# Optimization experiments

Measured on AMD Instinct MI355X. Metric: run time of the kernel, lower is better.

## Reference

```python
import jax, jax.numpy as jnp
import numpy as np

_SAMPLING_EPS = 1e-5
EOS_PROB_RATIO = 100.0
MIN_PROB_THRESHOLD = 0.001
MIX_RATIO = 0.5
EOS_TOKEN_ID = 2


def setup_inputs() -> dict:
    key = jax.random.key(0)
    k1, k2, k3, k4 = jax.random.split(key, 4)
    B, V = 256, 128000
    logits = jax.random.normal(k1, (B, V), dtype=jnp.float32) * 3.0
    # keep temperature away from 0 so the random-sampling path is exercised
    temperature = 0.2 + 1.3 * jax.random.uniform(k2, (B,), dtype=jnp.float32)
    top_p = 0.5 + 0.5 * jax.random.uniform(k3, (B,), dtype=jnp.float32)
    token_lengths = jax.random.randint(k4, (V,), 0, 20).astype(jnp.int32)
    return {
        "logits": logits,
        "temperature": temperature,
        "top_p": top_p,
        "token_lengths": token_lengths,
        "top_k": 50,
    }


def _apply_top_k_top_p(logits, top_k, top_p):
    """vLLM-style: ascending sort, top-k threshold, top-p cumulative mask, scatter back."""
    idx = jnp.argsort(logits, axis=-1)  # ascending
    lsort = jnp.take_along_axis(logits, idx, axis=-1)
    V = logits.shape[-1]
    # top-k: keep only the last top_k (largest) entries
    kth = lsort[:, V - top_k][:, None]
    lsort = jnp.where(lsort < kth, -jnp.inf, lsort)
    # top-p: mask low-cumulative-probability prefix (ascending order)
    probs = jax.nn.softmax(lsort, axis=-1)
    csum = jnp.cumsum(probs, axis=-1)
    pmask = csum <= (1.0 - top_p[:, None])
    pmask = pmask.at[:, -1].set(False)  # always keep the top token
    lsort = jnp.where(pmask, -jnp.inf, lsort)
    # scatter back to original token order
    inv = jnp.argsort(idx, axis=-1)
    return jnp.take_along_axis(lsort, inv, axis=-1)


def _longest_word_sample(logits, token_lengths, k, mix_ratio, eos_token_id):
    topk_logits, topk_idx = jax.lax.top_k(logits, k)  # [B,k]
    prob = jax.nn.softmax(topk_logits, axis=-1)
    lens = token_lengths[jnp.clip(topk_idx, 0, token_lengths.shape[0] - 1)].astype(jnp.float32)
    length_score = jax.nn.softmax(lens, axis=-1)
    mix = (1.0 - mix_ratio) * prob + mix_ratio * length_score
    mix = jnp.where(prob >= MIN_PROB_THRESHOLD, mix, -jnp.inf)
    # EOS threshold rule
    eos_in_topk = (topk_idx == eos_token_id) & jnp.isfinite(topk_logits)
    rows_with_eos = eos_in_topk.any(axis=-1, keepdims=True)
    eos_prob = jnp.sum(prob * eos_in_topk, axis=-1, keepdims=True)
    eos_thresh = jnp.maximum(eos_prob / EOS_PROB_RATIO, 0.005)
    valid = prob >= eos_thresh
    mix = jnp.where(valid | ~rows_with_eos, mix, -jnp.inf)
    best = jnp.argmax(mix, axis=-1)  # [B]
    chosen = jnp.take_along_axis(topk_idx, best[:, None], axis=-1)[:, 0]
    return chosen


def reference(logits, temperature, top_p, token_lengths, top_k):
    greedy = jnp.argmax(logits, axis=-1)
    scaled = logits / temperature[:, None]
    filtered = _apply_top_k_top_p(scaled, top_k, top_p)
    rnd = _longest_word_sample(filtered, token_lengths, top_k, MIX_RATIO, EOS_TOKEN_ID)
    sampled = jnp.where(temperature < _SAMPLING_EPS, greedy, rnd)
    return sampled.astype(jnp.int32)
```

## Files before the change

### kernel.cpp

```cpp
#include <hip/hip_runtime.h>
#include <stdint.h>
#include <math.h>

typedef unsigned long long u64;

#define K1_THREADS 512
#define K1_WAVES 8
#define K1_BATCH 4
#define SPLIT 4
#define NBINS 2048
#define BIN_SHIFT 21
#define CAND_MAX 1024
#define MAXK 64

__device__ __forceinline__ uint32_t fkey(float f) {
    uint32_t b = __float_as_uint(f);
    return b ^ (uint32_t)(((int32_t)b >> 31) | 0x80000000);
}
__device__ __forceinline__ float fval(uint32_t k) {
    uint32_t b = (k & 0x80000000u) ? (k & 0x7FFFFFFFu) : ~k;
    return __uint_as_float(b);
}

#define INSB(vf, gidx) do {                                                    \
    u64 c_ = ((u64)fkey(vf) << 32) | (uint32_t)~(uint32_t)(gidx);              \
    bool g0_ = c_ > t0; u64 n0_ = g0_ ? c_ : t0; c_ = g0_ ? t0 : c_; t0 = n0_; \
    bool g1_ = c_ > t1; u64 n1_ = g1_ ? c_ : t1; c_ = g1_ ? t1 : c_; t1 = n1_; \
    bool g2_ = c_ > t2; u64 n2_ = g2_ ? c_ : t2; c_ = g2_ ? t2 : c_; t2 = n2_; \
    bool g3_ = c_ > t3; u64 n3_ = g3_ ? c_ : t3; c_ = g3_ ? t3 : c_; t3 = n3_; \
    uint32_t dk_ = (uint32_t)(c_ >> 32);                                       \
    dkey = (dk_ > dkey) ? dk_ : dkey;                                          \
} while (0)

__global__ __launch_bounds__(K1_THREADS, 8) void topk_slice_kernel(
    const float* __restrict__ logits,
    const int* __restrict__ top_k_ptr,
    u64* __restrict__ ws, int V)
{
    const int row = blockIdx.x / SPLIT;
    const int sl  = blockIdx.x % SPLIT;
    const int tid = threadIdx.x;
    const int lane = tid & 63;
    const int wid  = tid >> 6;
    int K = *top_k_ptr;
    if (K < 1) K = 1;
    if (K > MAXK) K = MAXK;

    __shared__ u64 s_cand4[K1_THREADS * 4];
    __shared__ uint32_t s_hist[NBINS];
    __shared__ u64 s_cand[CAND_MAX];
    __shared__ u64 s_top[MAXK];
    __shared__ uint32_t s_wsum[K1_WAVES], s_wtail[K1_WAVES];
    __shared__ int s_T, s_cnt;

    for (int i = tid; i < NBINS; i += K1_THREADS) s_hist[i] = 0u;
    if (tid == 0) s_cnt = 0;

    const float* rowbase = logits + (size_t)row * (size_t)V;
    const float4* rowp = reinterpret_cast<const float4*>(rowbase);
    const int nv = V >> 2;
    const int snf = (nv + SPLIT - 1) / SPLIT;
    const int f0 = sl * snf;
    const int f1 = (f0 + snf < nv) ? (f0 + snf) : nv;

    u64 t0 = 0ull, t1 = 0ull, t2 = 0ull, t3 = 0ull;
    uint32_t dkey = 0u;
    const int step = K1_THREADS * K1_BATCH;
    const int niter = (f1 - f0) / step;

    for (int it = 0; it < niter; ++it) {
        const int j0 = f0 + it * step + tid;
        float4 x[K1_BATCH];
        #pragma unroll
        for (int b = 0; b < K1_BATCH; ++b) x[b] = rowp[j0 + b * K1_THREADS];
        #pragma unroll
        for (int b = 0; b < K1_BATCH; ++b) {
            const int g = (j0 + b * K1_THREADS) << 2;
            INSB(x[b].x, g + 0);
            INSB(x[b].y, g + 1);
            INSB(x[b].z, g + 2);
            INSB(x[b].w, g + 3);
        }
    }
    for (int j = f0 + niter * step + tid; j < f1; j += K1_THREADS) {
        float4 x = rowp[j];
        const int g = j << 2;
        INSB(x.x, g + 0);
        INSB(x.y, g + 1);
        INSB(x.z, g + 2);
        INSB(x.w, g + 3);
    }
    __syncthreads();

    s_cand4[tid * 4 + 0] = t0;
    s_cand4[tid * 4 + 1] = t1;
    s_cand4[tid * 4 + 2] = t2;
    s_cand4[tid * 4 + 3] = t3;
    atomicAdd(&s_hist[(uint32_t)(t0 >> 32) >> BIN_SHIFT], 1u);
    atomicAdd(&s_hist[(uint32_t)(t1 >> 32) >> BIN_SHIFT], 1u);
    atomicAdd(&s_hist[(uint32_t)(t2 >> 32) >> BIN_SHIFT], 1u);
    atomicAdd(&s_hist[(uint32_t)(t3 >> 32) >> BIN_SHIFT], 1u);
    __syncthreads();

    const int CH = NBINS / K1_THREADS;
    uint32_t cs = 0;
    {
        const int b0 = tid * CH;
        #pragma unroll
        for (int b = 0; b < CH; ++b) cs += s_hist[b0 + b];
    }
    uint32_t suf = cs;
    #pragma unroll
    for (int off = 1; off < 64; off <<= 1) {
        uint32_t o = __shfl_down(suf, off, 64);
        suf += (lane + off < 64) ? o : 0u;
    }
    if (lane == 0) s_wsum[wid] = suf;
    __syncthreads();
    if (wid == 0 && lane < K1_WAVES) {
        uint32_t t = s_wsum[lane];
        uint32_t s = t;
        #pragma unroll
        for (int off = 1; off < K1_WAVES; off <<= 1) {
            uint32_t o = __shfl_down(s, off, 64);
            s += (lane + off < K1_WAVES) ? o : 0u;
        }
        s_wtail[lane] = s - t;
    }
    __syncthreads();
    {
        uint32_t sufg = suf + s_wtail[wid];
        uint32_t sufn = sufg - cs;
        if (sufg >= (uint32_t)K && sufn < (uint32_t)K) {
            uint32_t acc = sufn;
            int T = tid * CH;
            for (int b = tid * CH + CH - 1; b >= tid * CH; --b) {
                acc += s_hist[b];
                if (acc >= (uint32_t)K) { T = b; break; }
            }
            s_T = T;
        }
    }
    __syncthreads();

    const uint32_t T = (uint32_t)s_T;
    #pragma unroll
    for (int r = 0; r < 4; ++r) {
        u64 c = s_cand4[tid * 4 + r];
        if (((uint32_t)(c >> 32) >> BIN_SHIFT) >= T) {
            int p = atomicAdd(&s_cnt, 1);
            if (p < CAND_MAX) s_cand[p] = c;
        }
    }
    __syncthreads();

    {
        const int M = (s_cnt < CAND_MAX) ? s_cnt : CAND_MAX;
        for (int t = tid; t < M; t += K1_THREADS) {
            const u64 mine = s_cand[t];
            int rank = 0;
            for (int j = 0; j < M; ++j) rank += (s_cand[j] > mine) ? 1 : 0;
            if (rank < MAXK) s_top[rank] = mine;
        }
    }
    __syncthreads();

    const u64 kth = s_top[K - 1];
    const int bad = (dkey >= (uint32_t)(kth >> 32)) ? 1 : 0;
    if (__syncthreads_or(bad)) {
        if (tid == 0) s_cnt = 0;
        __syncthreads();
        const int e0 = f0 << 2;
        const int e1 = f1 << 2;
        for (int e = e0 + tid; e < e1; e += K1_THREADS) {
            u64 p = ((u64)fkey(rowbase[e]) << 32) | (uint32_t)~(uint32_t)e;
            if (p >= kth) {
                int q = atomicAdd(&s_cnt, 1);
                if (q < CAND_MAX) s_cand[q] = p;
            }
        }
        __syncthreads();
        const int M2 = (s_cnt < CAND_MAX) ? s_cnt : CAND_MAX;
        for (int t = tid; t < M2; t += K1_THREADS) {
            const u64 mine = s_cand[t];
            int rank = 0;
            for (int j = 0; j < M2; ++j) rank += (s_cand[j] > mine) ? 1 : 0;
            if (rank < MAXK) s_top[rank] = mine;
        }
        __syncthreads();
    }

    if (tid < K) ws[(size_t)blockIdx.x * MAXK + tid] = s_top[tid];
}

__global__ __launch_bounds__(256) void merge_sampler_kernel(
    const u64* __restrict__ ws,
    const float* __restrict__ temperature,
    const float* __restrict__ top_p,
    const int* __restrict__ token_lengths,
    const int* __restrict__ top_k_ptr,
    int* __restrict__ out, int V)
{
    const int row = blockIdx.x;
    const int tid = threadIdx.x;
    int K = *top_k_ptr;
    if (K < 1) K = 1;
    if (K > MAXK) K = MAXK;
    const int M = SPLIT * K;

    __shared__ u64 s_cand[SPLIT * MAXK];
    __shared__ float s_vals[MAXK];
    __shared__ int s_idx[MAXK], s_slot[MAXK];

    if (tid < M) {
        const int s = tid / K, k = tid - s * K;
        s_cand[tid] = ws[(size_t)(row * SPLIT + s) * MAXK + k];
    }
    __syncthreads();

    if (tid < M) {
        const u64 mine = s_cand[tid];
        int rank = 0;
        for (int j = 0; j < M; ++j) rank += (s_cand[j] > mine) ? 1 : 0;
        if (rank < MAXK) {
            s_idx[rank]  = (int)(~(uint32_t)mine);
            s_vals[rank] = fval((uint32_t)(mine >> 32));
        }
    }
    __syncthreads();

    if (tid >= 64) return;

    const float temp = temperature[row];
    const float tp   = top_p[row];

    const float a0 = s_vals[0] / temp;
    float e = 0.f;
    int myidx = -1;
    if (tid < K) {
        myidx = s_idx[tid];
        e = expf(s_vals[tid] / temp - a0);
    }
    float sum = e;
    #pragma unroll
    for (int off = 1; off < 64; off <<= 1) sum += __shfl_xor(sum, off, 64);
    const float p1 = e / sum;

    float csf = p1;
    #pragma unroll
    for (int off = 1; off < 64; off <<= 1) {
        float o = __shfl_down(csf, off, 64);
        csf += (tid + off < 64) ? o : 0.f;
    }
    const float lim = 1.0f - tp;
    const bool keep = (tid < K) && (tid == 0 || csf > lim);
    const int S = __popcll(__ballot(keep));

    float e2 = (tid < S) ? e : 0.f;
    float sum2 = e2;
    #pragma unroll
    for (int off = 1; off < 64; off <<= 1) sum2 += __shfl_xor(sum2, off, 64);
    const float p2 = e2 / sum2;

    const bool is_eos = (tid < S) && (myidx == 2);
    float eosp = is_eos ? p2 : 0.f;
    #pragma unroll
    for (int off = 1; off < 64; off <<= 1) eosp += __shfl_xor(eosp, off, 64);
    const bool has_eos = (__ballot(is_eos) != 0ull);
    const float eth = fmaxf(eosp / 100.0f, 0.005f);

    if (tid < S) s_slot[tid] = myidx;
    __builtin_amdgcn_wave_barrier();
    if (tid == 0) {
        u64 m0 = 0ull, m1 = 0ull;
        for (int i = 0; i < S; ++i) {
            int id = s_idx[i];
            if (id < 64) m0 |= 1ull << id;
            else if (id < 128) m1 |= 1ull << (id - 64);
        }
        int nxt = 0;
        for (int i = S; i < K; ++i) {
            while ((nxt < 64) ? ((m0 >> nxt) & 1ull) : ((m1 >> (nxt - 64)) & 1ull)) nxt++;
            s_slot[i] = nxt++;
        }
    }
    __builtin_amdgcn_wave_barrier();

    float len = -INFINITY;
    if (tid < K) {
        int id = s_slot[tid];
        id = (id < 0) ? 0 : ((id >= V) ? V - 1 : id);
        len = (float)token_lengths[id];
    }
    float lmax = len;
    #pragma unroll
    for (int off = 1; off < 64; off <<= 1) lmax = fmaxf(lmax, __shfl_xor(lmax, off, 64));
    float el = (tid < K) ? expf(len - lmax) : 0.f;
    float lsum = el;
    #pragma unroll
    for (int off = 1; off < 64; off <<= 1) lsum += __shfl_xor(lsum, off, 64);
    const float ls = el / lsum;

    float mix = -INFINITY;
    if (tid < S) {
        mix = 0.5f * p2 + 0.5f * ls;
        if (!(p2 >= 0.001f)) mix = -INFINITY;
        if (has_eos && !(p2 >= eth)) mix = -INFINITY;
    }
    float bm = mix; int bi = tid;
    #pragma unroll
    for (int off = 1; off < 64; off <<= 1) {
        float om = __shfl_xor(bm, off, 64);
        int   oi = __shfl_xor(bi, off, 64);
        if (om > bm || (om == bm && oi < bi)) { bm = om; bi = oi; }
    }

    if (tid == 0) {
        int chosen = s_slot[bi];
        if (temp < 1e-5f) chosen = s_idx[0];
        out[row] = chosen;
    }
}

extern "C" void kernel_launch(void* const* d_in, const int* in_sizes, int n_in,
                              void* d_out, int out_size, void* d_ws, size_t ws_size,
                              hipStream_t stream) {
    const float* logits        = (const float*)d_in[0];
    const float* temperature   = (const float*)d_in[1];
    const float* top_p         = (const float*)d_in[2];
    const int*   token_lengths = (const int*)d_in[3];
    const int*   top_k_ptr     = (const int*)d_in[4];
    int* outp = (int*)d_out;
    u64* ws   = (u64*)d_ws;

    const int B = in_sizes[1];
    const int V = in_sizes[3];

    topk_slice_kernel<<<B * SPLIT, K1_THREADS, 0, stream>>>(logits, top_k_ptr, ws, V);
    merge_sampler_kernel<<<B, 256, 0, stream>>>(ws, temperature, top_p,
                                                token_lengths, top_k_ptr, outp, V);
}
```

Baseline: 49.64 us.

## Replace per-thread top-4 insertion with sampled histogram threshold and filter pass

Each block now builds a histogram from a small strided sample of its slice and picks a bin threshold so that about SAMPLE_TARGET sampled values lie above it. A single streaming pass then pushes every element above the threshold into a shared candidate list, and the threshold is adjusted one bin at a time and the pass repeated if too few or too many candidates appear. This removes the register sorting network run on every element, at the risk of several full re-scans when the sample is unrepresentative. After the retry limit, rows can end up with fewer than K candidates or with the list truncated, which could drop true top-k entries.

```diff
diff --git a/kernel.cpp b/kernel.cpp
--- a/kernel.cpp
+++ b/kernel.cpp
@@ -10,7 +10,8 @@
 #define SPLIT 4
 #define NBINS 2048
 #define BIN_SHIFT 21
-#define CAND_MAX 1024
+#define SAMPLE_TARGET 16
+#define CAND_MAX 2048
 #define MAXK 64
 
 __device__ __forceinline__ uint32_t fkey(float f) {
@@ -21,16 +22,6 @@
     uint32_t b = (k & 0x80000000u) ? (k & 0x7FFFFFFFu) : ~k;
     return __uint_as_float(b);
 }
-
-#define INSB(vf, gidx) do {                                                    \
-    u64 c_ = ((u64)fkey(vf) << 32) | (uint32_t)~(uint32_t)(gidx);              \
-    bool g0_ = c_ > t0; u64 n0_ = g0_ ? c_ : t0; c_ = g0_ ? t0 : c_; t0 = n0_; \
-    bool g1_ = c_ > t1; u64 n1_ = g1_ ? c_ : t1; c_ = g1_ ? t1 : c_; t1 = n1_; \
-    bool g2_ = c_ > t2; u64 n2_ = g2_ ? c_ : t2; c_ = g2_ ? t2 : c_; t2 = n2_; \
-    bool g3_ = c_ > t3; u64 n3_ = g3_ ? c_ : t3; c_ = g3_ ? t3 : c_; t3 = n3_; \
-    uint32_t dk_ = (uint32_t)(c_ >> 32);                                       \
-    dkey = (dk_ > dkey) ? dk_ : dkey;                                          \
-} while (0)
 
 __global__ __launch_bounds__(K1_THREADS, 8) void topk_slice_kernel(
     const float* __restrict__ logits,
@@ -46,7 +37,6 @@
     if (K < 1) K = 1;
     if (K > MAXK) K = MAXK;
 
-    __shared__ u64 s_cand4[K1_THREADS * 4];
     __shared__ uint32_t s_hist[NBINS];
     __shared__ u64 s_cand[CAND_MAX];
     __shared__ u64 s_top[MAXK];
@@ -54,7 +44,6 @@
     __shared__ int s_T, s_cnt;
 
     for (int i = tid; i < NBINS; i += K1_THREADS) s_hist[i] = 0u;
-    if (tid == 0) s_cnt = 0;
 
     const float* rowbase = logits + (size_t)row * (size_t)V;
     const float4* rowp = reinterpret_cast<const float4*>(rowbase);
@@ -62,44 +51,19 @@
     const int snf = (nv + SPLIT - 1) / SPLIT;
     const int f0 = sl * snf;
     const int f1 = (f0 + snf < nv) ? (f0 + snf) : nv;
-
-    u64 t0 = 0ull, t1 = 0ull, t2 = 0ull, t3 = 0ull;
-    uint32_t dkey = 0u;
-    const int step = K1_THREADS * K1_BATCH;
-    const int niter = (f1 - f0) / step;
-
-    for (int it = 0; it < niter; ++it) {
-        const int j0 = f0 + it * step + tid;
-        float4 x[K1_BATCH];
-        #pragma unroll
-        for (int b = 0; b < K1_BATCH; ++b) x[b] = rowp[j0 + b * K1_THREADS];
-        #pragma unroll
-        for (int b = 0; b < K1_BATCH; ++b) {
-            const int g = (j0 + b * K1_THREADS) << 2;
-            INSB(x[b].x, g + 0);
-            INSB(x[b].y, g + 1);
-            INSB(x[b].z, g + 2);
-            INSB(x[b].w, g + 3);
-        }
-    }
-    for (int j = f0 + niter * step + tid; j < f1; j += K1_THREADS) {
+    __syncthreads();
+
+    {
+        int stride = (f1 - f0) / K1_THREADS;
+        if (stride < 1) stride = 1;
+        int j = f0 + tid * stride;
+        if (j >= f1) j = f1 - 1;
         float4 x = rowp[j];
-        const int g = j << 2;
-        INSB(x.x, g + 0);
-        INSB(x.y, g + 1);
-        INSB(x.z, g + 2);
-        INSB(x.w, g + 3);
-    }
-    __syncthreads();
-
-    s_cand4[tid * 4 + 0] = t0;
-    s_cand4[tid * 4 + 1] = t1;
-    s_cand4[tid * 4 + 2] = t2;
-    s_cand4[tid * 4 + 3] = t3;
-    atomicAdd(&s_hist[(uint32_t)(t0 >> 32) >> BIN_SHIFT], 1u);
-    atomicAdd(&s_hist[(uint32_t)(t1 >> 32) >> BIN_SHIFT], 1u);
-    atomicAdd(&s_hist[(uint32_t)(t2 >> 32) >> BIN_SHIFT], 1u);
-    atomicAdd(&s_hist[(uint32_t)(t3 >> 32) >> BIN_SHIFT], 1u);
+        atomicAdd(&s_hist[fkey(x.x) >> BIN_SHIFT], 1u);
+        atomicAdd(&s_hist[fkey(x.y) >> BIN_SHIFT], 1u);
+        atomicAdd(&s_hist[fkey(x.z) >> BIN_SHIFT], 1u);
+        atomicAdd(&s_hist[fkey(x.w) >> BIN_SHIFT], 1u);
+    }
     __syncthreads();
 
     const int CH = NBINS / K1_THREADS;
@@ -131,64 +95,74 @@
     {
         uint32_t sufg = suf + s_wtail[wid];
         uint32_t sufn = sufg - cs;
-        if (sufg >= (uint32_t)K && sufn < (uint32_t)K) {
+        if (sufg >= (uint32_t)SAMPLE_TARGET && sufn < (uint32_t)SAMPLE_TARGET) {
             uint32_t acc = sufn;
             int T = tid * CH;
             for (int b = tid * CH + CH - 1; b >= tid * CH; --b) {
                 acc += s_hist[b];
-                if (acc >= (uint32_t)K) { T = b; break; }
+                if (acc >= (uint32_t)SAMPLE_TARGET) { T = b; break; }
             }
             s_T = T;
         }
     }
     __syncthreads();
 
-    const uint32_t T = (uint32_t)s_T;
-    #pragma unroll
-    for (int r = 0; r < 4; ++r) {
-        u64 c = s_cand4[tid * 4 + r];
-        if (((uint32_t)(c >> 32) >> BIN_SHIFT) >= T) {
-            int p = atomicAdd(&s_cnt, 1);
-            if (p < CAND_MAX) s_cand[p] = c;
-        }
-    }
-    __syncthreads();
-
-    {
-        const int M = (s_cnt < CAND_MAX) ? s_cnt : CAND_MAX;
-        for (int t = tid; t < M; t += K1_THREADS) {
-            const u64 mine = s_cand[t];
-            int rank = 0;
-            for (int j = 0; j < M; ++j) rank += (s_cand[j] > mine) ? 1 : 0;
-            if (rank < MAXK) s_top[rank] = mine;
-        }
-    }
-    __syncthreads();
-
-    const u64 kth = s_top[K - 1];
-    const int bad = (dkey >= (uint32_t)(kth >> 32)) ? 1 : 0;
-    if (__syncthreads_or(bad)) {
+    int T = s_T;
+    int M = 0;
+    const int step = K1_THREADS * K1_BATCH;
+    const int niter = (f1 - f0) / step;
+
+    #define FILT(vf, gidx) do {                                                \
+        uint32_t k_ = fkey(vf);                                                \
+        if ((int)(k_ >> BIN_SHIFT) >= T) {                                     \
+            int p_ = atomicAdd(&s_cnt, 1);                                     \
+            if (p_ < CAND_MAX)                                                 \
+                s_cand[p_] = ((u64)k_ << 32) | (uint32_t)~(uint32_t)(gidx);    \
+        }                                                                      \
+    } while (0)
+
+    for (int attempt = 0; ; ++attempt) {
+        __syncthreads();
         if (tid == 0) s_cnt = 0;
         __syncthreads();
-        const int e0 = f0 << 2;
-        const int e1 = f1 << 2;
-        for (int e = e0 + tid; e < e1; e += K1_THREADS) {
-            u64 p = ((u64)fkey(rowbase[e]) << 32) | (uint32_t)~(uint32_t)e;
-            if (p >= kth) {
-                int q = atomicAdd(&s_cnt, 1);
-                if (q < CAND_MAX) s_cand[q] = p;
+
+        for (int it = 0; it < niter; ++it) {
+            const int j0 = f0 + it * step + tid;
+            float4 x[K1_BATCH];
+            #pragma unroll
+            for (int b = 0; b < K1_BATCH; ++b) x[b] = rowp[j0 + b * K1_THREADS];
+            #pragma unroll
+            for (int b = 0; b < K1_BATCH; ++b) {
+                const int g = (j0 + b * K1_THREADS) << 2;
+                FILT(x[b].x, g + 0);
+                FILT(x[b].y, g + 1);
+                FILT(x[b].z, g + 2);
+                FILT(x[b].w, g + 3);
             }
         }
+        for (int j = f0 + niter * step + tid; j < f1; j += K1_THREADS) {
+            float4 x = rowp[j];
+            const int g = j << 2;
+            FILT(x.x, g + 0);
+            FILT(x.y, g + 1);
+            FILT(x.z, g + 2);
+            FILT(x.w, g + 3);
+        }
         __syncthreads();
-        const int M2 = (s_cnt < CAND_MAX) ? s_cnt : CAND_MAX;
-        for (int t = tid; t < M2; t += K1_THREADS) {
-            const u64 mine = s_cand[t];
-            int rank = 0;
-            for (int j = 0; j < M2; ++j) rank += (s_cand[j] > mine) ? 1 : 0;
-            if (rank < MAXK) s_top[rank] = mine;
-        }
-        __syncthreads();
-    }
+        M = s_cnt;
+        if ((M >= K && M <= CAND_MAX) || attempt >= 11) break;
+        T += (M < K) ? -1 : 1;
+        if (T < 0) T = 0;
+    }
+    if (M > CAND_MAX) M = CAND_MAX;
+
+    for (int t = tid; t < M; t += K1_THREADS) {
+        const u64 mine = s_cand[t];
+        int rank = 0;
+        for (int j = 0; j < M; ++j) rank += (s_cand[j] > mine) ? 1 : 0;
+        if (rank < MAXK) s_top[rank] = mine;
+    }
+    __syncthreads();
 
     if (tid < K) ws[(size_t)blockIdx.x * MAXK + tid] = s_top[tid];
 }
```

After: 76.47 us. 1.54x slower.

## Replace per-thread top-4 insertion with sampled-threshold ballot filtering

Applied to the files above, without the earlier changes.

Instead of keeping a per-thread sorted top-4 via compare-swap chains, the kernel first samples one float4 per thread to build a histogram and picks a threshold bin. It then streams the slice and compacts elements above that threshold into per-wave shared segments using ballot and popcount, retrying with an adjusted threshold on overflow or underflow. The old top-4 path remains as a fallback. This is meant to cut the per-element ALU cost of the insertion network, but a bad threshold costs extra full passes over the slice.

```diff
diff --git a/kernel.cpp b/kernel.cpp
--- a/kernel.cpp
+++ b/kernel.cpp
@@ -10,7 +10,9 @@
 #define SPLIT 4
 #define NBINS 2048
 #define BIN_SHIFT 21
-#define CAND_MAX 1024
+#define SAMPLE_TARGET 16
+#define WSEG 256
+#define CAND_TOT (K1_WAVES * WSEG)
 #define MAXK 64
 
 __device__ __forceinline__ uint32_t fkey(float f) {
@@ -30,6 +32,21 @@
     bool g3_ = c_ > t3; u64 n3_ = g3_ ? c_ : t3; c_ = g3_ ? t3 : c_; t3 = n3_; \
     uint32_t dk_ = (uint32_t)(c_ >> 32);                                       \
     dkey = (dk_ > dkey) ? dk_ : dkey;                                          \
+} while (0)
+
+#define ELEM(vf, gidx) do {                                                    \
+    uint32_t k_ = fkey(vf);                                                    \
+    bool hit_ = inb_ && ((int)(k_ >> BIN_SHIFT) >= T);                         \
+    u64 m_ = __ballot(hit_);                                                   \
+    if (m_) {                                                                  \
+        if (hit_) {                                                            \
+            int pos_ = wcnt + __popcll(m_ & lanemask_lt);                      \
+            if (pos_ < WSEG)                                                   \
+                s_cand[wid * WSEG + pos_] =                                    \
+                    ((u64)k_ << 32) | (uint32_t)~(uint32_t)(gidx);             \
+        }                                                                      \
+        wcnt += (int)__popcll(m_);                                             \
+    }                                                                          \
 } while (0)
 
 __global__ __launch_bounds__(K1_THREADS, 8) void topk_slice_kernel(
@@ -46,15 +63,14 @@
     if (K < 1) K = 1;
     if (K > MAXK) K = MAXK;
 
-    __shared__ u64 s_cand4[K1_THREADS * 4];
     __shared__ uint32_t s_hist[NBINS];
-    __shared__ u64 s_cand[CAND_MAX];
+    __shared__ u64 s_cand[CAND_TOT];
     __shared__ u64 s_top[MAXK];
     __shared__ uint32_t s_wsum[K1_WAVES], s_wtail[K1_WAVES];
+    __shared__ int s_wcnt[K1_WAVES];
     __shared__ int s_T, s_cnt;
 
     for (int i = tid; i < NBINS; i += K1_THREADS) s_hist[i] = 0u;
-    if (tid == 0) s_cnt = 0;
 
     const float* rowbase = logits + (size_t)row * (size_t)V;
     const float4* rowp = reinterpret_cast<const float4*>(rowbase);
@@ -62,44 +78,20 @@
     const int snf = (nv + SPLIT - 1) / SPLIT;
     const int f0 = sl * snf;
     const int f1 = (f0 + snf < nv) ? (f0 + snf) : nv;
-
-    u64 t0 = 0ull, t1 = 0ull, t2 = 0ull, t3 = 0ull;
-    uint32_t dkey = 0u;
-    const int step = K1_THREADS * K1_BATCH;
-    const int niter = (f1 - f0) / step;
-
-    for (int it = 0; it < niter; ++it) {
-        const int j0 = f0 + it * step + tid;
-        float4 x[K1_BATCH];
-        #pragma unroll
-        for (int b = 0; b < K1_BATCH; ++b) x[b] = rowp[j0 + b * K1_THREADS];
-        #pragma unroll
-        for (int b = 0; b < K1_BATCH; ++b) {
-            const int g = (j0 + b * K1_THREADS) << 2;
-            INSB(x[b].x, g + 0);
-            INSB(x[b].y, g + 1);
-            INSB(x[b].z, g + 2);
-            INSB(x[b].w, g + 3);
-        }
-    }
-    for (int j = f0 + niter * step + tid; j < f1; j += K1_THREADS) {
+    const int fcl = f1 - 1;
+    __syncthreads();
+
+    {
+        int stride = (f1 - f0) / K1_THREADS;
+        if (stride < 1) stride = 1;
+        int j = f0 + tid * stride;
+        if (j > fcl) j = fcl;
         float4 x = rowp[j];
-        const int g = j << 2;
-        INSB(x.x, g + 0);
-        INSB(x.y, g + 1);
-        INSB(x.z, g + 2);
-        INSB(x.w, g + 3);
-    }
-    __syncthreads();
-
-    s_cand4[tid * 4 + 0] = t0;
-    s_cand4[tid * 4 + 1] = t1;
-    s_cand4[tid * 4 + 2] = t2;
-    s_cand4[tid * 4 + 3] = t3;
-    atomicAdd(&s_hist[(uint32_t)(t0 >> 32) >> BIN_SHIFT], 1u);
-    atomicAdd(&s_hist[(uint32_t)(t1 >> 32) >> BIN_SHIFT], 1u);
-    atomicAdd(&s_hist[(uint32_t)(t2 >> 32) >> BIN_SHIFT], 1u);
-    atomicAdd(&s_hist[(uint32_t)(t3 >> 32) >> BIN_SHIFT], 1u);
+        atomicAdd(&s_hist[fkey(x.x) >> BIN_SHIFT], 1u);
+        atomicAdd(&s_hist[fkey(x.y) >> BIN_SHIFT], 1u);
+        atomicAdd(&s_hist[fkey(x.z) >> BIN_SHIFT], 1u);
+        atomicAdd(&s_hist[fkey(x.w) >> BIN_SHIFT], 1u);
+    }
     __syncthreads();
 
     const int CH = NBINS / K1_THREADS;
@@ -131,63 +123,134 @@
     {
         uint32_t sufg = suf + s_wtail[wid];
         uint32_t sufn = sufg - cs;
-        if (sufg >= (uint32_t)K && sufn < (uint32_t)K) {
+        if (sufg >= (uint32_t)SAMPLE_TARGET && sufn < (uint32_t)SAMPLE_TARGET) {
             uint32_t acc = sufn;
             int T = tid * CH;
             for (int b = tid * CH + CH - 1; b >= tid * CH; --b) {
                 acc += s_hist[b];
-                if (acc >= (uint32_t)K) { T = b; break; }
+                if (acc >= (uint32_t)SAMPLE_TARGET) { T = b; break; }
             }
             s_T = T;
         }
     }
     __syncthreads();
 
-    const uint32_t T = (uint32_t)s_T;
-    #pragma unroll
-    for (int r = 0; r < 4; ++r) {
-        u64 c = s_cand4[tid * 4 + r];
-        if (((uint32_t)(c >> 32) >> BIN_SHIFT) >= T) {
-            int p = atomicAdd(&s_cnt, 1);
-            if (p < CAND_MAX) s_cand[p] = c;
-        }
-    }
-    __syncthreads();
-
-    {
-        const int M = (s_cnt < CAND_MAX) ? s_cnt : CAND_MAX;
-        for (int t = tid; t < M; t += K1_THREADS) {
+    int T = s_T;
+    const int step = K1_THREADS * K1_BATCH;
+    const int niter = (f1 - f0 + step - 1) / step;
+    const u64 lanemask_lt = (1ull << lane) - 1ull;
+
+    bool ok = false;
+    for (int attempt = 0; attempt < 6 && !ok; ++attempt) {
+        int wcnt = 0;
+        for (int it = 0; it < niter; ++it) {
+            const int j0 = f0 + it * step + tid;
+            float4 x[K1_BATCH];
+            #pragma unroll
+            for (int b = 0; b < K1_BATCH; ++b) {
+                int j = j0 + b * K1_THREADS;
+                x[b] = rowp[(j < fcl) ? j : fcl];
+            }
+            #pragma unroll
+            for (int b = 0; b < K1_BATCH; ++b) {
+                const int j = j0 + b * K1_THREADS;
+                const bool inb_ = (j < f1);
+                const int g = j << 2;
+                ELEM(x[b].x, g + 0);
+                ELEM(x[b].y, g + 1);
+                ELEM(x[b].z, g + 2);
+                ELEM(x[b].w, g + 3);
+            }
+        }
+        if (lane == 0) s_wcnt[wid] = wcnt;
+        __syncthreads();
+        int tot = 0;
+        bool ovf = false;
+        for (int w = 0; w < K1_WAVES; ++w) {
+            int c = s_wcnt[w];
+            ovf |= (c > WSEG);
+            tot += (c > WSEG) ? WSEG : c;
+        }
+        __syncthreads();
+        if (!ovf && tot >= K) ok = true;
+        else T += ovf ? 1 : -1;
+        if (T < 0) T = 0;
+    }
+
+    if (ok) {
+        for (int slot = tid; slot < CAND_TOT; slot += K1_THREADS) {
+            const int w = slot >> 8, i = slot & (WSEG - 1);
+            if (i < s_wcnt[w]) {
+                const u64 mine = s_cand[slot];
+                int rank = 0;
+                for (int w2 = 0; w2 < K1_WAVES; ++w2) {
+                    const int c2 = s_wcnt[w2];
+                    const u64* seg = &s_cand[w2 * WSEG];
+                    for (int jj = 0; jj < c2; ++jj) rank += (seg[jj] > mine) ? 1 : 0;
+                }
+                if (rank < MAXK) s_top[rank] = mine;
+            }
+        }
+        __syncthreads();
+    } else {
+        u64 t0 = 0ull, t1 = 0ull, t2 = 0ull, t3 = 0ull;
+        uint32_t dkey = 0u;
+        for (int it = 0; it < niter; ++it) {
+            const int j0 = f0 + it * step + tid;
+            float4 x[K1_BATCH];
+            #pragma unroll
+            for (int b = 0; b < K1_BATCH; ++b) {
+                int j = j0 + b * K1_THREADS;
+                x[b] = rowp[(j < fcl) ? j : fcl];
+            }
+            #pragma unroll
+            for (int b = 0; b < K1_BATCH; ++b) {
+                const int j = j0 + b * K1_THREADS;
+                if (j < f1) {
+                    const int g = j << 2;
+                    INSB(x[b].x, g + 0);
+                    INSB(x[b].y, g + 1);
+                    INSB(x[b].z, g + 2);
+                    INSB(x[b].w, g + 3);
+                }
+            }
+        }
+        __syncthreads();
+        s_cand[tid * 4 + 0] = t0;
+        s_cand[tid * 4 + 1] = t1;
+        s_cand[tid * 4 + 2] = t2;
+        s_cand[tid * 4 + 3] = t3;
+        __syncthreads();
+        for (int t = tid; t < CAND_TOT; t += K1_THREADS) {
             const u64 mine = s_cand[t];
             int rank = 0;
-            for (int j = 0; j < M; ++j) rank += (s_cand[j] > mine) ? 1 : 0;
+            for (int jj = 0; jj < CAND_TOT; ++jj) rank += (s_cand[jj] > mine) ? 1 : 0;
             if (rank < MAXK) s_top[rank] = mine;
         }
-    }
-    __syncthreads();
-
-    const u64 kth = s_top[K - 1];
-    const int bad = (dkey >= (uint32_t)(kth >> 32)) ? 1 : 0;
-    if (__syncthreads_or(bad)) {
-        if (tid == 0) s_cnt = 0;
-        __syncthreads();
-        const int e0 = f0 << 2;
-        const int e1 = f1 << 2;
-        for (int e = e0 + tid; e < e1; e += K1_THREADS) {
-            u64 p = ((u64)fkey(rowbase[e]) << 32) | (uint32_t)~(uint32_t)e;
-            if (p >= kth) {
-                int q = atomicAdd(&s_cnt, 1);
-                if (q < CAND_MAX) s_cand[q] = p;
-            }
-        }
-        __syncthreads();
-        const int M2 = (s_cnt < CAND_MAX) ? s_cnt : CAND_MAX;
-        for (int t = tid; t < M2; t += K1_THREADS) {
-            const u64 mine = s_cand[t];
-            int rank = 0;
-            for (int j = 0; j < M2; ++j) rank += (s_cand[j] > mine) ? 1 : 0;
-            if (rank < MAXK) s_top[rank] = mine;
-        }
-        __syncthreads();
+        __syncthreads();
+        const u64 kth = s_top[K - 1];
+        const int bad = (dkey >= (uint32_t)(kth >> 32)) ? 1 : 0;
+        if (__syncthreads_or(bad)) {
+            if (tid == 0) s_cnt = 0;
+            __syncthreads();
+            const int e0 = f0 << 2, e1 = f1 << 2;
+            for (int e = e0 + tid; e < e1; e += K1_THREADS) {
+                u64 p = ((u64)fkey(rowbase[e]) << 32) | (uint32_t)~(uint32_t)e;
+                if (p >= kth) {
+                    int q = atomicAdd(&s_cnt, 1);
+                    if (q < CAND_TOT) s_cand[q] = p;
+                }
+            }
+            __syncthreads();
+            const int M2 = (s_cnt < CAND_TOT) ? s_cnt : CAND_TOT;
+            for (int t = tid; t < M2; t += K1_THREADS) {
+                const u64 mine = s_cand[t];
+                int rank = 0;
+                for (int jj = 0; jj < M2; ++jj) rank += (s_cand[jj] > mine) ? 1 : 0;
+                if (rank < MAXK) s_top[rank] = mine;
+            }
+            __syncthreads();
+        }
     }
 
     if (tid < K) ws[(size_t)blockIdx.x * MAXK + tid] = s_top[tid];
```

New measurement: 112.0 us. 126% more time.
